# Kernel tuning notes

Hardware: AMD Instinct MI355X
Metric: run time of the kernel (lower is better)

Reference implementation:

```python
import jax, jax.numpy as jnp
import numpy as np
from jax import lax

FEAT_STRIDE = 16
PRE_NMS_TOP_N = 6000   # cfg['TEST'].RPN_PRE_NMS_TOP_N
POST_NMS_TOP_N = 300   # cfg['TEST'].RPN_POST_NMS_TOP_N
NMS_THRESH = 0.7       # cfg['TEST'].RPN_NMS_THRESH
MIN_SIZE = 16.0        # cfg['TEST'].RPN_MIN_SIZE
B, A, H, W = 32, 9, 128, 128
NEG_INF = jnp.float32(-1e30)


def _whctrs(a):
    w = a[2] - a[0] + 1.0
    h = a[3] - a[1] + 1.0
    return w, h, a[0] + 0.5 * (w - 1), a[1] + 0.5 * (h - 1)

def _mkanchors(ws, hs, xc, yc):
    ws = ws[:, None]; hs = hs[:, None]
    return np.hstack((xc - 0.5 * (ws - 1), yc - 0.5 * (hs - 1),
                      xc + 0.5 * (ws - 1), yc + 0.5 * (hs - 1)))

def _ratio_enum(anchor, ratios):
    w, h, xc, yc = _whctrs(anchor)
    size = w * h
    ws = np.round(np.sqrt(size / ratios))
    hs = np.round(ws * ratios)
    return _mkanchors(ws, hs, xc, yc)

def _scale_enum(anchor, scales):
    w, h, xc, yc = _whctrs(anchor)
    return _mkanchors(w * scales, h * scales, xc, yc)

def generate_anchors(base_size=16, ratios=np.array([0.5, 1.0, 2.0]), scales=np.array([8.0, 16.0, 32.0])):
    base = np.array([1, 1, base_size, base_size], dtype=np.float64) - 1
    ra = _ratio_enum(base, ratios)
    return np.vstack([_scale_enum(ra[i], scales) for i in range(ra.shape[0])]).astype(np.float32)

_BASE_ANCHORS = generate_anchors()  # (A, 4)

def _all_anchors(h, w):
    sx = np.arange(w) * FEAT_STRIDE
    sy = np.arange(h) * FEAT_STRIDE
    sx, sy = np.meshgrid(sx, sy)  # row-major (h, w) matches permute(0,2,3,1) ordering
    shifts = np.stack([sx.ravel(), sy.ravel(), sx.ravel(), sy.ravel()], axis=1).astype(np.float32)
    return jnp.asarray((shifts[:, None, :] + _BASE_ANCHORS[None, :, :]).reshape(-1, 4))  # (h*w*A, 4)

# ---- bbox_transform_inv / clip_boxes ----

def _decode(anchors, deltas):
    ws = anchors[:, 2] - anchors[:, 0] + 1.0
    hs = anchors[:, 3] - anchors[:, 1] + 1.0
    cx = anchors[:, 0] + 0.5 * ws
    cy = anchors[:, 1] + 0.5 * hs
    dx, dy, dw, dh = deltas[:, 0], deltas[:, 1], deltas[:, 2], deltas[:, 3]
    pcx = dx * ws + cx
    pcy = dy * hs + cy
    pw = jnp.exp(dw) * ws
    ph = jnp.exp(dh) * hs
    return jnp.stack([pcx - 0.5 * pw, pcy - 0.5 * ph, pcx + 0.5 * pw, pcy + 0.5 * ph], axis=1)

def _clip(b, imh, imw):
    x1 = jnp.clip(b[:, 0], 0.0, imw - 1.0)
    y1 = jnp.clip(b[:, 1], 0.0, imh - 1.0)
    x2 = jnp.clip(b[:, 2], 0.0, imw - 1.0)
    y2 = jnp.clip(b[:, 3], 0.0, imh - 1.0)
    return jnp.stack([x1, y1, x2, y2], axis=1)

# ---- greedy NMS: pick top-score box, suppress IoU > thresh, repeat POST times ----

def _nms_select(boxes, scores):
    # boxes: (PRE, 4) score-sorted; scores: (PRE,)
    areas = (boxes[:, 2] - boxes[:, 0] + 1.0) * (boxes[:, 3] - boxes[:, 1] + 1.0)

    def body(i, st):
        s, keep, valid = st
        j = jnp.argmax(s)
        keep = keep.at[i].set(j)
        valid = valid.at[i].set(s[j] > NEG_INF)
        b = boxes[j]
        xx1 = jnp.maximum(b[0], boxes[:, 0])
        yy1 = jnp.maximum(b[1], boxes[:, 1])
        xx2 = jnp.minimum(b[2], boxes[:, 2])
        yy2 = jnp.minimum(b[3], boxes[:, 3])
        inter = jnp.maximum(xx2 - xx1 + 1.0, 0.0) * jnp.maximum(yy2 - yy1 + 1.0, 0.0)
        iou = inter / jnp.maximum(areas[j] + areas - inter, 1e-6)
        s = jnp.where(iou > NMS_THRESH, NEG_INF, s)  # suppresses j itself (IoU = 1)
        return s, keep, valid

    init = (scores, jnp.zeros((POST_NMS_TOP_N,), jnp.int32), jnp.zeros((POST_NMS_TOP_N,), bool))
    _, keep, valid = lax.fori_loop(0, POST_NMS_TOP_N, body, init)
    return keep, valid

def _per_image(sc, dl, info, anchors):
    prop = _clip(_decode(anchors, dl), info[0], info[1])  # (K*A, 4)
    ws = prop[:, 2] - prop[:, 0] + 1.0
    hs = prop[:, 3] - prop[:, 1] + 1.0
    min_sz = MIN_SIZE * info[2]
    sc = jnp.where((ws >= min_sz) & (hs >= min_sz), sc, NEG_INF)
    top_s, top_i = lax.top_k(sc, PRE_NMS_TOP_N)
    cand = prop[top_i]  # (PRE, 4)
    keep, valid = _nms_select(cand, top_s)
    return cand[keep] * valid[:, None].astype(cand.dtype)  # zero-pad invalid rows

def _forward(rpn_cls_prob, rpn_bbox_pred, im_info):
    b, _, h, w = rpn_cls_prob.shape
    anchors = _all_anchors(h, w)
    scores = rpn_cls_prob[:, A:, :, :].transpose(0, 2, 3, 1).reshape(b, -1)  # (b, h*w*A)
    deltas = rpn_bbox_pred.transpose(0, 2, 3, 1).reshape(b, -1, 4)           # (b, h*w*A, 4)
    boxes = jax.vmap(lambda s, d, i: _per_image(s, d, i, anchors))(scores, deltas, im_info)
    ids = jnp.broadcast_to(jnp.arange(b, dtype=boxes.dtype)[:, None, None], (b, POST_NMS_TOP_N, 1))
    return jnp.concatenate([ids, boxes], axis=2)  # (b, POST, 5): [batch_idx, x1, y1, x2, y2]

def setup_inputs() -> dict:
    key = jax.random.key(0)
    k1, k2 = jax.random.split(key)
    rpn_cls_prob = jax.random.uniform(k1, (B, 2 * A, H, W), dtype=jnp.float32)
    rpn_bbox_pred = jax.random.normal(k2, (B, 4 * A, H, W), dtype=jnp.float32) * 0.2
    im_info = jnp.tile(jnp.array([[H * FEAT_STRIDE, W * FEAT_STRIDE, 1.0]], dtype=jnp.float32), (B, 1))
    return {"rpn_cls_prob": rpn_cls_prob, "rpn_bbox_pred": rpn_bbox_pred, "im_info": im_info}

def reference(rpn_cls_prob, rpn_bbox_pred, im_info):
    return _forward(rpn_cls_prob, rpn_bbox_pred, im_info)
```

## Files before the change

kernel.cpp:

```cpp
#include <hip/hip_runtime.h>
#include <cstdint>
#include <cstddef>

#pragma clang fp contract(off)

typedef unsigned long long u64;

#define NB 32
#define NA 9
#define NH 128
#define NW 128
#define HW (NH*NW)
#define NANCH (NA*HW)
#define PRE_N 6000
#define POST_N 300
#define CAND_CAP 8192
#define NMS_T 0.7f
#define GX_GATHER 24
#define NBOX 6144
#define CH 512

__constant__ float c_wa[9] = {184.f,368.f,736.f,128.f,256.f,512.f,88.f,176.f,352.f};
__constant__ float c_ha[9] = {96.f,192.f,384.f,128.f,256.f,512.f,176.f,352.f,704.f};

__device__ __forceinline__ float4 decode_clip(int a, int h, int w,
    float dx, float dy, float dlw, float dlh, float imh, float imw) {
  float wa = c_wa[a], ha = c_ha[a];
  float cx = (float)w * 16.0f + 8.0f;
  float cy = (float)h * 16.0f + 8.0f;
  float pcx = dx * wa + cx;
  float pcy = dy * ha + cy;
  float pw = expf(dlw) * wa;
  float ph = expf(dlh) * ha;
  float x1 = pcx - 0.5f * pw;
  float y1 = pcy - 0.5f * ph;
  float x2 = pcx + 0.5f * pw;
  float y2 = pcy + 0.5f * ph;
  float4 r;
  r.x = fminf(fmaxf(x1, 0.0f), imw - 1.0f);
  r.y = fminf(fmaxf(y1, 0.0f), imh - 1.0f);
  r.z = fminf(fmaxf(x2, 0.0f), imw - 1.0f);
  r.w = fminf(fmaxf(y2, 0.0f), imh - 1.0f);
  return r;
}

__device__ __forceinline__ unsigned score_key(float sc, float bw, float bh, float msz) {
  unsigned bits = __float_as_uint(sc);
  unsigned key = (bits & 0x80000000u) ? ~bits : (bits | 0x80000000u);
  if (!(bw >= msz && bh >= msz)) key = 0u;
  return key;
}

__device__ __forceinline__ bool sup_test4(float4 v, float ar, float4 p, float pa) {
  float xx1 = fmaxf(p.x, v.x), yy1 = fmaxf(p.y, v.y);
  float xx2 = fminf(p.z, v.z), yy2 = fminf(p.w, v.w);
  float iw = fmaxf(xx2 - xx1 + 1.0f, 0.0f);
  float ih = fmaxf(yy2 - yy1 + 1.0f, 0.0f);
  float inter = iw * ih;
  float iou = inter / fmaxf(pa + ar - inter, 1e-6f);
  return iou > NMS_T;
}

__device__ __forceinline__ u64 shfl_xor_u64(u64 x, int m) {
  int lo = __shfl_xor((int)(unsigned)x, m, 64);
  int hi = __shfl_xor((int)(unsigned)(x >> 32), m, 64);
  return ((u64)(unsigned)hi << 32) | (unsigned)lo;
}

__device__ __forceinline__ void reg_step(u64 v[8], int t, int k, int j) {
  #pragma unroll
  for (int r = 0; r < 8; ++r) {
    if ((r & j) == 0) {
      int e = (t << 3) + r;
      bool up = ((e & k) == 0);
      u64 x = v[r], y = v[r | j];
      u64 mx = x > y ? x : y, mn = x > y ? y : x;
      v[r]     = up ? mx : mn;
      v[r | j] = up ? mn : mx;
    }
  }
}

__device__ __forceinline__ void shfl_step(u64 v[8], int t, int k, int j) {
  int m = j >> 3;
  bool lower = ((t & m) == 0);
  #pragma unroll
  for (int r = 0; r < 8; ++r) {
    int e = (t << 3) + r;
    bool up = ((e & k) == 0);
    u64 pv = shfl_xor_u64(v[r], m);
    bool keepmax = (up == lower);
    u64 x = v[r];
    u64 mx = x > pv ? x : pv, mn = x > pv ? pv : x;
    v[r] = keepmax ? mx : mn;
  }
}

__device__ __forceinline__ void lds_step(u64* sm, u64 v[8], int t, int k, int j) {
  int m = j >> 3;
  __syncthreads();
  #pragma unroll
  for (int r = 0; r < 8; ++r) sm[(r << 10) | t] = v[r];
  __syncthreads();
  bool lower = ((t & m) == 0);
  bool up = (((t << 3) & k) == 0);
  bool keepmax = (up == lower);
  int pt = t ^ m;
  #pragma unroll
  for (int r = 0; r < 8; ++r) {
    u64 pv = sm[(r << 10) | pt];
    u64 x = v[r];
    u64 mx = x > pv ? x : pv, mn = x > pv ? pv : x;
    v[r] = keepmax ? mx : mn;
  }
}

__device__ void find_B(const unsigned* __restrict__ hb, unsigned* part,
                       unsigned* outB, unsigned* outCum) {
  int tid = threadIdx.x;
  unsigned s = 0;
  for (int i = 0; i < 16; ++i) s += hb[tid*16 + i];
  part[tid] = s;
  __syncthreads();
  for (int off = 1; off < 256; off <<= 1) {
    unsigned v = (tid + off < 256) ? part[tid + off] : 0u;
    __syncthreads();
    part[tid] += v;
    __syncthreads();
  }
  unsigned St = part[tid];
  unsigned Sn = (tid < 255) ? part[tid + 1] : 0u;
  if (St >= (unsigned)PRE_N && Sn < (unsigned)PRE_N) {
    unsigned cum = Sn, B = 0, cumAbove = Sn;
    for (int i = 15; i >= 0; --i) {
      unsigned v = hb[tid*16 + i];
      if (cum + v >= (unsigned)PRE_N) { B = (unsigned)(tid*16 + i); cumAbove = cum; break; }
      cum += v;
    }
    *outB = B; *outCum = cumAbove;
  }
  __syncthreads();
}

__device__ void find_thr(const unsigned* __restrict__ hb2, unsigned B, unsigned cum0,
                         unsigned* part, unsigned* outThr) {
  int tid = threadIdx.x;
  unsigned s = 0;
  for (int i = 0; i < 16; ++i) s += hb2[tid*16 + i];
  part[tid] = s;
  __syncthreads();
  for (int off = 1; off < 256; off <<= 1) {
    unsigned v = (tid + off < 256) ? part[tid + off] : 0u;
    __syncthreads();
    part[tid] += v;
    __syncthreads();
  }
  unsigned St = cum0 + part[tid];
  unsigned Sn = cum0 + ((tid < 255) ? part[tid + 1] : 0u);
  if (St >= (unsigned)PRE_N && Sn < (unsigned)PRE_N) {
    unsigned cum = Sn, t = 1u;
    for (int i = 15; i >= 0; --i) {
      unsigned v = hb2[tid*16 + i];
      if (cum + v >= (unsigned)PRE_N) {
        t = (B << 20) | ((unsigned)(tid*16 + i) << 8);
        break;
      }
      cum += v;
    }
    if (t == 0u) t = 1u;
    *outThr = t;
  }
  __syncthreads();
}

__global__ __launch_bounds__(256) void k_keys(const float* __restrict__ cls,
    const float* __restrict__ dl, const float* __restrict__ info,
    unsigned* __restrict__ keys, unsigned* __restrict__ hist) {
  __shared__ unsigned hsh[4096];
  int tid = threadIdx.x;
  for (int i = tid; i < 4096; i += 256) hsh[i] = 0;
  int t = blockIdx.x * 256 + tid;
  int b = blockIdx.y;
  int hw0 = t * 4;
  int h = hw0 >> 7;
  const float* dlb  = dl  + (size_t)b * (4*NA*HW);
  const float* clsb = cls + (size_t)b * (2*NA*HW);
  float imh = info[b*3+0], imw = info[b*3+1];
  float msz = 16.0f * info[b*3+2];
  unsigned* kb = keys + (size_t)b * NANCH;
  __syncthreads();
  #pragma unroll
  for (int a = 0; a < 9; ++a) {
    float4 dx4 = *(const float4*)&dlb[(a*4+0)*HW + hw0];
    float4 dy4 = *(const float4*)&dlb[(a*4+1)*HW + hw0];
    float4 dw4 = *(const float4*)&dlb[(a*4+2)*HW + hw0];
    float4 dh4 = *(const float4*)&dlb[(a*4+3)*HW + hw0];
    float4 sc4 = *(const float4*)&clsb[(NA+a)*HW + hw0];
    uint4 out;
    {
      float4 bx = decode_clip(a, h, (hw0+0)&127, dx4.x, dy4.x, dw4.x, dh4.x, imh, imw);
      out.x = score_key(sc4.x, bx.z-bx.x+1.0f, bx.w-bx.y+1.0f, msz);
    }
    {
      float4 bx = decode_clip(a, h, (hw0+1)&127, dx4.y, dy4.y, dw4.y, dh4.y, imh, imw);
      out.y = score_key(sc4.y, bx.z-bx.x+1.0f, bx.w-bx.y+1.0f, msz);
    }
    {
      float4 bx = decode_clip(a, h, (hw0+2)&127, dx4.z, dy4.z, dw4.z, dh4.z, imh, imw);
      out.z = score_key(sc4.z, bx.z-bx.x+1.0f, bx.w-bx.y+1.0f, msz);
    }
    {
      float4 bx = decode_clip(a, h, (hw0+3)&127, dx4.w, dy4.w, dw4.w, dh4.w, imh, imw);
      out.w = score_key(sc4.w, bx.z-bx.x+1.0f, bx.w-bx.y+1.0f, msz);
    }
    *(uint4*)&kb[a*HW + hw0] = out;
    atomicAdd(&hsh[out.x >> 20], 1u);
    atomicAdd(&hsh[out.y >> 20], 1u);
    atomicAdd(&hsh[out.z >> 20], 1u);
    atomicAdd(&hsh[out.w >> 20], 1u);
  }
  __syncthreads();
  unsigned* gb = hist + ((size_t)b << 12);
  for (int i = tid; i < 4096; i += 256) {
    unsigned v = hsh[i];
    if (v) atomicAdd(&gb[i], v);
  }
}

__global__ __launch_bounds__(256) void k_hist2(const unsigned* __restrict__ keys,
    const unsigned* __restrict__ hist1, unsigned* __restrict__ hist2) {
  __shared__ unsigned h[4096];
  __shared__ unsigned part[256];
  __shared__ unsigned sB, sCum;
  int b = blockIdx.y, tid = threadIdx.x;
  for (int i = tid; i < 4096; i += 256) h[i] = 0;
  __syncthreads();
  find_B(hist1 + ((size_t)b << 12), part, &sB, &sCum);
  unsigned B = sB;
  const unsigned* kb = keys + (size_t)b * NANCH;
  for (int i = blockIdx.x * 256 + tid; i < NANCH; i += gridDim.x * 256) {
    unsigned k = kb[i];
    if ((k >> 20) == B) atomicAdd(&h[(k >> 8) & 4095u], 1u);
  }
  __syncthreads();
  unsigned* gb = hist2 + ((size_t)b << 12);
  for (int i = tid; i < 4096; i += 256) { unsigned v = h[i]; if (v) atomicAdd(&gb[i], v); }
}

__global__ __launch_bounds__(256) void k_gather(const unsigned* __restrict__ keys,
    const unsigned* __restrict__ hist1, const unsigned* __restrict__ hist2,
    const float* __restrict__ dl, const float* __restrict__ info,
    unsigned* __restrict__ cnt, u64* __restrict__ cand,
    float4* __restrict__ boxes) {
  int b = blockIdx.y, tid = threadIdx.x;
  int lane = tid & 63, wv = tid >> 6;
  __shared__ unsigned part[256];
  __shared__ unsigned sB, sCum, sThr;
  __shared__ unsigned wcnt[4], woff[4], blkbase;
  if (tid == 0) sThr = 1u;
  __syncthreads();
  find_B(hist1 + ((size_t)b << 12), part, &sB, &sCum);
  find_thr(hist2 + ((size_t)b << 12), sB, sCum, part, &sThr);
  unsigned t_ = sThr;
  const unsigned* kb = keys + (size_t)b * NANCH;
  const float* dlb = dl + (size_t)b * (4*NA*HW);
  float imh = info[b*3+0], imw = info[b*3+1];
  u64* cb = cand + (size_t)b * CAND_CAP;
  float4* bxc = boxes + (size_t)b * CAND_CAP;
  unsigned* cp = cnt + (size_t)b * 64;
  const int PER_BLK = NANCH / GX_GATHER;
  int base0 = blockIdx.x * PER_BLK;
  for (int it = 0; it < PER_BLK / 256; ++it) {
    int j = base0 + it * 256 + tid;
    unsigned key = kb[j];
    bool pass = key >= t_;
    u64 mask = __ballot(pass);
    if (lane == 0) wcnt[wv] = (unsigned)__popcll(mask);
    __syncthreads();
    if (tid == 0) {
      unsigned s0 = 0;
      for (int w = 0; w < 4; ++w) { woff[w] = s0; s0 += wcnt[w]; }
      blkbase = s0 ? atomicAdd(cp, s0) : 0u;
    }
    __syncthreads();
    if (pass) {
      unsigned pos = blkbase + woff[wv] + (unsigned)__popcll(mask & ((1ull << lane) - 1ull));
      if (pos < CAND_CAP) {
        int a = j >> 14, hw = j & (HW - 1);
        unsigned oi = (unsigned)(hw * 9 + a);
        unsigned noi = (~oi) & 0x3FFFFu;
        cb[pos] = ((u64)key << 32) | ((u64)noi << 13) | (u64)pos;
        bxc[pos] = decode_clip(a, hw >> 7, hw & 127,
                               dlb[(a*4+0)*HW + hw], dlb[(a*4+1)*HW + hw],
                               dlb[(a*4+2)*HW + hw], dlb[(a*4+3)*HW + hw],
                               imh, imw);
      }
    }
    __syncthreads();
  }
}

__global__ __launch_bounds__(1024) void k_final5(const u64* __restrict__ cand,
    const unsigned* __restrict__ cnt, const float4* __restrict__ boxes,
    float* __restrict__ out) {
  __shared__ float4 bx[NBOX];
  __shared__ float4 cbox2[CH];
  __shared__ float  carea2[CH];
  __shared__ float4 kbox[POST_N];
  __shared__ float  karea[POST_N];
  __shared__ u64 sup[CH][9];
  __shared__ u64 aliveM[8];
  __shared__ u64 kgW[8];
  __shared__ int s_nk;
  u64* sm = (u64*)bx;

  int b = blockIdx.x, tid = threadIdx.x;
  int lane = tid & 63, wv = tid >> 6;
  if (tid == 0) s_nk = 0;

  unsigned effcnt = cnt[b * 64];
  if (effcnt > CAND_CAP) effcnt = CAND_CAP;
  const u64* cb = cand + (size_t)b * CAND_CAP;
  int e0 = tid << 3;
  u64 v[8];
  #pragma unroll
  for (int r = 0; r < 8; ++r)
    v[r] = ((unsigned)(e0 + r) < effcnt) ? cb[e0 + r] : 0ull;

  for (int k = 2; k <= 8; k <<= 1)
    for (int j = k >> 1; j >= 1; j >>= 1) reg_step(v, tid, k, j);
  for (int k = 16; k <= CAND_CAP; k <<= 1) {
    int j = k >> 1;
    for (; j >= 512; j >>= 1) lds_step(sm, v, tid, k, j);
    for (; j >= 8;   j >>= 1) shfl_step(v, tid, k, j);
    for (; j >= 1;   j >>= 1) reg_step(v, tid, k, j);
  }
  __syncthreads();

  const float4* bxc = boxes + (size_t)b * CAND_CAP;
  #pragma unroll
  for (int r = 0; r < 8; ++r) {
    int rank = e0 + r;
    if (rank < NBOX) {
      u64 ck = (rank < PRE_N) ? v[r] : 0ull;
      float4 w = make_float4(0.f, 0.f, -1.f, -1.f);
      if ((unsigned)(ck >> 32) != 0u)
        w = bxc[(unsigned)(ck & 0x1FFFu)];
      bx[rank] = w;
    }
  }
  __syncthreads();

  float* ob = out + (size_t)b * (POST_N * 5);
  int c = tid & (CH - 1);
  int seg = tid >> 9;

  for (int base = 0; base < NBOX; base += CH) {
    int nk0 = s_nk;

    bool alive = false;
    float4 w; float ar = 0.f;
    if (tid < CH) {
      w = bx[base + tid];
      float wid = w.z - w.x + 1.0f;
      alive = wid > 0.0f;
      ar = wid * (w.w - w.y + 1.0f);
      if (alive) {
        for (int k = 0; k < nk0; ++k) {
          if (sup_test4(w, ar, kbox[k], karea[k])) { alive = false; break; }
        }
      }
      u64 am = __ballot(alive);
      if (lane == 0) aliveM[wv] = am;
    }
    __syncthreads();

    int na = 0;
    #pragma unroll
    for (int g = 0; g < 8; ++g) na += (int)__popcll(aliveM[g]);
    if (na == 0) continue;

    if (tid < CH && alive) {
      int cg2 = tid >> 6;
      int pre = 0;
      #pragma unroll
      for (int g = 0; g < 8; ++g) if (g < cg2) pre += (int)__popcll(aliveM[g]);
      pre += (int)__popcll(aliveM[cg2] & ((1ull << (tid & 63)) - 1ull));
      cbox2[pre] = w;
      carea2[pre] = ar;
    }
    __syncthreads();

    {
      int i = c;
      if (i < na) {
        int ngi = (i >> 6) + 1;
        int gA = seg ? (ngi >> 1) : 0;
        int gB = seg ? ngi : (ngi >> 1);
        if (gA < gB) {
          float4 vi = cbox2[i];
          float ai = carea2[i];
          for (int g = gA; g < gB; ++g) {
            int jmax = i - (g << 6);
            if (jmax > 64) jmax = 64;
            u64 r = 0;
            #pragma unroll 4
            for (int j = 0; j < jmax; ++j) {
              if (sup_test4(vi, ai, cbox2[(g << 6) + j], carea2[(g << 6) + j]))
                r |= 1ull << j;
            }
            sup[i][g] = r;
          }
        }
      }
    }
    __syncthreads();

    if (tid < 64) {
      u64 kw[8];
      int nst = (na + 63) >> 6;
      u64 srow[8];
      {
        const u64* rp = sup[lane];
        #pragma unroll
        for (int g = 0; g < 8; ++g) srow[g] = rp[g];
      }
      #pragma unroll
      for (int s = 0; s < 8; ++s) {
        u64 nsr[8];
        bool pf = (s + 1 < nst);
        if (pf) {
          const u64* rp = sup[(s + 1) * 64 + lane];
          #pragma unroll
          for (int g = 0; g < 8; ++g) nsr[g] = rp[g];
        }
        u64 kg = 0;
        if (s < nst) {
          int cc = s * 64 + lane;
          bool a = (cc < na);
          u64 blocked = 0;
          #pragma unroll
          for (int g = 0; g < 8; ++g) if (g < s) blocked |= (srow[g] & kw[g]);
          a = a && (blocked == 0ull);
          u64 r = a ? srow[s] : 0ull;
          u64 cm = __ballot(a);
          while (cm) {
            int j = __builtin_ctzll(cm);
            kg |= 1ull << j;
            u64 rem = __ballot((r >> j) & 1ull);
            cm &= ~(rem | (1ull << j));
          }
        }
        kw[s] = kg;
        if (pf) {
          #pragma unroll
          for (int g = 0; g < 8; ++g) srow[g] = nsr[g];
        }
      }
      if (lane == 0) {
        #pragma unroll
        for (int s = 0; s < 8; ++s) kgW[s] = kw[s];
      }
    }
    __syncthreads();

    if (tid < na) {
      int s = tid >> 6;
      u64 kgw = kgW[s];
      bool kept = (kgw >> (tid & 63)) & 1;
      int pre = 0;
      #pragma unroll
      for (int g = 0; g < 8; ++g) if (g < s) pre += (int)__popcll(kgW[g]);
      pre += (int)__popcll(kgw & ((1ull << (tid & 63)) - 1ull));
      int rank = nk0 + pre;
      if (kept && rank < POST_N) {
        float4 ww = cbox2[tid];
        kbox[rank] = ww; karea[rank] = carea2[tid];
        ob[rank*5+0] = (float)b;
        ob[rank*5+1] = ww.x; ob[rank*5+2] = ww.y; ob[rank*5+3] = ww.z; ob[rank*5+4] = ww.w;
      }
    }
    if (tid == 0) {
      int tot = 0;
      #pragma unroll
      for (int s = 0; s < 8; ++s) tot += (int)__popcll(kgW[s]);
      int nn = nk0 + tot;
      s_nk = nn < POST_N ? nn : POST_N;
    }
    __syncthreads();
    if (s_nk >= POST_N) break;
  }
  __syncthreads();
  int nk = s_nk;
  for (int r = nk + tid; r < POST_N; r += 1024) {
    ob[r*5+0] = (float)b;
    ob[r*5+1] = 0.f; ob[r*5+2] = 0.f; ob[r*5+3] = 0.f; ob[r*5+4] = 0.f;
  }
}

extern "C" void kernel_launch(void* const* d_in, const int* in_sizes, int n_in,
                              void* d_out, int out_size, void* d_ws, size_t ws_size,
                              hipStream_t stream) {
  const float* cls  = (const float*)d_in[0];
  const float* dl   = (const float*)d_in[1];
  const float* info = (const float*)d_in[2];
  float* out = (float*)d_out;
  char* ws = (char*)d_ws;

  const size_t OFF_KEYS = 0;
  const size_t OFF_H1   = 18874368;
  const size_t OFF_H2   = 19398656;
  const size_t OFF_CNT  = 19922944;
  const size_t OFF_CAND = 19931136;
  const size_t OFF_BOX  = 22028288;
  const size_t WS_NEED  = 26222592;
  if (ws_size < WS_NEED) return;

  unsigned* keys  = (unsigned*)(ws + OFF_KEYS);
  unsigned* h1    = (unsigned*)(ws + OFF_H1);
  unsigned* h2    = (unsigned*)(ws + OFF_H2);
  unsigned* cnt   = (unsigned*)(ws + OFF_CNT);
  u64* cand = (u64*)(ws + OFF_CAND);
  float4* boxes = (float4*)(ws + OFF_BOX);

  hipMemsetAsync(ws + OFF_H1, 0, OFF_CAND - OFF_H1, stream);

  dim3 g1(HW / 1024, NB);
  k_keys<<<g1, 256, 0, stream>>>(cls, dl, info, keys, h1);
  dim3 gh(8, NB);
  k_hist2<<<gh, 256, 0, stream>>>(keys, h1, h2);
  dim3 gg(GX_GATHER, NB);
  k_gather<<<gg, 256, 0, stream>>>(keys, h1, h2, dl, info, cnt, cand, boxes);
  k_final5<<<NB, 1024, 0, stream>>>(cand, cnt, boxes, out);
}
```

Measured before the change: 330.5 us.

## Eagerly suppress future NMS chunks against newly kept boxes across all threads

The chunked NMS kernel used to test each 512-box chunk against every previously kept box serially, and only 512 threads did that work. Now each of the 1024 threads holds 6 candidate boxes in registers with a dead mask. After each chunk, all threads test their future boxes only against the boxes just kept, so the suppression work is spread over the whole block and is incremental. The cost is more registers per thread (six float4 boxes plus areas), which may cause spilling at 1024 threads, and redundant tests on boxes that would never be reached once 300 are kept.

```diff
diff --git a/kernel.cpp b/kernel.cpp
--- a/kernel.cpp
+++ b/kernel.cpp
@@ -300,7 +300,7 @@
   }
 }
 
-__global__ __launch_bounds__(1024) void k_final5(const u64* __restrict__ cand,
+__global__ __launch_bounds__(1024) void k_final6(const u64* __restrict__ cand,
     const unsigned* __restrict__ cnt, const float4* __restrict__ boxes,
     float* __restrict__ out) {
   __shared__ float4 bx[NBOX];
@@ -351,144 +351,170 @@
   }
   __syncthreads();
 
+  float4 mybx[6];
+  float  myar[6];
+  int deadm = 0;
+  #pragma unroll
+  for (int m = 0; m < 6; ++m) {
+    float4 w = bx[tid + (m << 10)];
+    mybx[m] = w;
+    float wid = w.z - w.x + 1.0f;
+    myar[m] = wid * (w.w - w.y + 1.0f);
+    if (!(wid > 0.0f)) deadm |= (1 << m);
+  }
+
   float* ob = out + (size_t)b * (POST_N * 5);
-  int c = tid & (CH - 1);
+  int c512 = tid & (CH - 1);
   int seg = tid >> 9;
-
-  for (int base = 0; base < NBOX; base += CH) {
-    int nk0 = s_nk;
-
-    bool alive = false;
-    float4 w; float ar = 0.f;
-    if (tid < CH) {
-      w = bx[base + tid];
-      float wid = w.z - w.x + 1.0f;
-      alive = wid > 0.0f;
-      ar = wid * (w.w - w.y + 1.0f);
+  bool done = false;
+
+  #pragma unroll
+  for (int m = 0; m < 6; ++m) {
+    #pragma unroll
+    for (int par = 0; par < 2; ++par) {
+      if (done) continue;
+      int nk0 = s_nk;
+
+      bool own = (tid >> 9) == par;
+      int cc = tid - (par << 9);
+      bool alive = own && !((deadm >> m) & 1);
+      {
+        u64 am = __ballot(alive);
+        if (own && lane == 0) aliveM[wv & 7] = am;
+      }
+      __syncthreads();
+
+      int na = 0;
+      #pragma unroll
+      for (int g = 0; g < 8; ++g) na += (int)__popcll(aliveM[g]);
+      if (na == 0) continue;
+
       if (alive) {
-        for (int k = 0; k < nk0; ++k) {
-          if (sup_test4(w, ar, kbox[k], karea[k])) { alive = false; break; }
-        }
-      }
-      u64 am = __ballot(alive);
-      if (lane == 0) aliveM[wv] = am;
-    }
-    __syncthreads();
-
-    int na = 0;
-    #pragma unroll
-    for (int g = 0; g < 8; ++g) na += (int)__popcll(aliveM[g]);
-    if (na == 0) continue;
-
-    if (tid < CH && alive) {
-      int cg2 = tid >> 6;
-      int pre = 0;
-      #pragma unroll
-      for (int g = 0; g < 8; ++g) if (g < cg2) pre += (int)__popcll(aliveM[g]);
-      pre += (int)__popcll(aliveM[cg2] & ((1ull << (tid & 63)) - 1ull));
-      cbox2[pre] = w;
-      carea2[pre] = ar;
-    }
-    __syncthreads();
-
-    {
-      int i = c;
-      if (i < na) {
-        int ngi = (i >> 6) + 1;
-        int gA = seg ? (ngi >> 1) : 0;
-        int gB = seg ? ngi : (ngi >> 1);
-        if (gA < gB) {
-          float4 vi = cbox2[i];
-          float ai = carea2[i];
-          for (int g = gA; g < gB; ++g) {
-            int jmax = i - (g << 6);
-            if (jmax > 64) jmax = 64;
-            u64 r = 0;
-            #pragma unroll 4
-            for (int j = 0; j < jmax; ++j) {
-              if (sup_test4(vi, ai, cbox2[(g << 6) + j], carea2[(g << 6) + j]))
-                r |= 1ull << j;
+        int cg2 = cc >> 6;
+        int pre = 0;
+        #pragma unroll
+        for (int g = 0; g < 8; ++g) if (g < cg2) pre += (int)__popcll(aliveM[g]);
+        pre += (int)__popcll(aliveM[cg2] & ((1ull << (cc & 63)) - 1ull));
+        cbox2[pre] = mybx[m];
+        carea2[pre] = myar[m];
+      }
+      __syncthreads();
+
+      {
+        int i = c512;
+        if (i < na) {
+          int ngi = (i >> 6) + 1;
+          int gA = seg ? (ngi >> 1) : 0;
+          int gB = seg ? ngi : (ngi >> 1);
+          if (gA < gB) {
+            float4 vi = cbox2[i];
+            float ai = carea2[i];
+            for (int g = gA; g < gB; ++g) {
+              int jmax = i - (g << 6);
+              if (jmax > 64) jmax = 64;
+              u64 r = 0;
+              #pragma unroll 4
+              for (int j = 0; j < jmax; ++j) {
+                if (sup_test4(vi, ai, cbox2[(g << 6) + j], carea2[(g << 6) + j]))
+                  r |= 1ull << j;
+              }
+              sup[i][g] = r;
             }
-            sup[i][g] = r;
           }
         }
       }
-    }
-    __syncthreads();
-
-    if (tid < 64) {
-      u64 kw[8];
-      int nst = (na + 63) >> 6;
-      u64 srow[8];
-      {
-        const u64* rp = sup[lane];
+      __syncthreads();
+
+      if (tid < 64) {
+        u64 kw[8];
+        int nst = (na + 63) >> 6;
+        u64 srow[8];
+        {
+          const u64* rp = sup[lane];
+          #pragma unroll
+          for (int g = 0; g < 8; ++g) srow[g] = rp[g];
+        }
         #pragma unroll
-        for (int g = 0; g < 8; ++g) srow[g] = rp[g];
-      }
-      #pragma unroll
-      for (int s = 0; s < 8; ++s) {
-        u64 nsr[8];
-        bool pf = (s + 1 < nst);
-        if (pf) {
-          const u64* rp = sup[(s + 1) * 64 + lane];
-          #pragma unroll
-          for (int g = 0; g < 8; ++g) nsr[g] = rp[g];
-        }
-        u64 kg = 0;
-        if (s < nst) {
-          int cc = s * 64 + lane;
-          bool a = (cc < na);
-          u64 blocked = 0;
-          #pragma unroll
-          for (int g = 0; g < 8; ++g) if (g < s) blocked |= (srow[g] & kw[g]);
-          a = a && (blocked == 0ull);
-          u64 r = a ? srow[s] : 0ull;
-          u64 cm = __ballot(a);
-          while (cm) {
-            int j = __builtin_ctzll(cm);
-            kg |= 1ull << j;
-            u64 rem = __ballot((r >> j) & 1ull);
-            cm &= ~(rem | (1ull << j));
+        for (int s = 0; s < 8; ++s) {
+          u64 nsr[8];
+          bool pf = (s + 1 < nst);
+          if (pf) {
+            const u64* rp = sup[(s + 1) * 64 + lane];
+            #pragma unroll
+            for (int g = 0; g < 8; ++g) nsr[g] = rp[g];
+          }
+          u64 kg = 0;
+          if (s < nst) {
+            int cc2 = s * 64 + lane;
+            bool a = (cc2 < na);
+            u64 blocked = 0;
+            #pragma unroll
+            for (int g = 0; g < 8; ++g) if (g < s) blocked |= (srow[g] & kw[g]);
+            a = a && (blocked == 0ull);
+            u64 r = a ? srow[s] : 0ull;
+            u64 cm = __ballot(a);
+            while (cm) {
+              int j = __builtin_ctzll(cm);
+              kg |= 1ull << j;
+              u64 rem = __ballot((r >> j) & 1ull);
+              cm &= ~(rem | (1ull << j));
+            }
+          }
+          kw[s] = kg;
+          if (pf) {
+            #pragma unroll
+            for (int g = 0; g < 8; ++g) srow[g] = nsr[g];
           }
         }
-        kw[s] = kg;
-        if (pf) {
+        if (lane == 0) {
           #pragma unroll
-          for (int g = 0; g < 8; ++g) srow[g] = nsr[g];
+          for (int s = 0; s < 8; ++s) kgW[s] = kw[s];
         }
       }
-      if (lane == 0) {
+      __syncthreads();
+
+      if (tid < na) {
+        int s = tid >> 6;
+        u64 kgw = kgW[s];
+        bool kept = (kgw >> (tid & 63)) & 1;
+        int pre = 0;
         #pragma unroll
-        for (int s = 0; s < 8; ++s) kgW[s] = kw[s];
-      }
-    }
-    __syncthreads();
-
-    if (tid < na) {
-      int s = tid >> 6;
-      u64 kgw = kgW[s];
-      bool kept = (kgw >> (tid & 63)) & 1;
-      int pre = 0;
-      #pragma unroll
-      for (int g = 0; g < 8; ++g) if (g < s) pre += (int)__popcll(kgW[g]);
-      pre += (int)__popcll(kgw & ((1ull << (tid & 63)) - 1ull));
-      int rank = nk0 + pre;
-      if (kept && rank < POST_N) {
-        float4 ww = cbox2[tid];
-        kbox[rank] = ww; karea[rank] = carea2[tid];
-        ob[rank*5+0] = (float)b;
-        ob[rank*5+1] = ww.x; ob[rank*5+2] = ww.y; ob[rank*5+3] = ww.z; ob[rank*5+4] = ww.w;
-      }
-    }
-    if (tid == 0) {
-      int tot = 0;
-      #pragma unroll
-      for (int s = 0; s < 8; ++s) tot += (int)__popcll(kgW[s]);
-      int nn = nk0 + tot;
-      s_nk = nn < POST_N ? nn : POST_N;
-    }
-    __syncthreads();
-    if (s_nk >= POST_N) break;
+        for (int g = 0; g < 8; ++g) if (g < s) pre += (int)__popcll(kgW[g]);
+        pre += (int)__popcll(kgw & ((1ull << (tid & 63)) - 1ull));
+        int rank = nk0 + pre;
+        if (kept && rank < POST_N) {
+          float4 ww = cbox2[tid];
+          kbox[rank] = ww; karea[rank] = carea2[tid];
+          ob[rank*5+0] = (float)b;
+          ob[rank*5+1] = ww.x; ob[rank*5+2] = ww.y; ob[rank*5+3] = ww.z; ob[rank*5+4] = ww.w;
+        }
+      }
+      if (tid == 0) {
+        int tot = 0;
+        #pragma unroll
+        for (int s = 0; s < 8; ++s) tot += (int)__popcll(kgW[s]);
+        int nn = nk0 + tot;
+        s_nk = nn < POST_N ? nn : POST_N;
+      }
+      __syncthreads();
+
+      int nk1 = s_nk;
+      if (nk1 >= POST_N) { done = true; continue; }
+      if (nk1 > nk0) {
+        #pragma unroll
+        for (int m2 = m; m2 < 6; ++m2) {
+          bool fut = (m2 > m) || ((tid >> 9) > par);
+          if (fut && !((deadm >> m2) & 1)) {
+            for (int k = nk0; k < nk1; ++k) {
+              if (sup_test4(mybx[m2], myar[m2], kbox[k], karea[k])) {
+                deadm |= (1 << m2);
+                break;
+              }
+            }
+          }
+        }
+      }
+    }
   }
   __syncthreads();
   int nk = s_nk;
@@ -531,5 +557,5 @@
   k_hist2<<<gh, 256, 0, stream>>>(keys, h1, h2);
   dim3 gg(GX_GATHER, NB);
   k_gather<<<gg, 256, 0, stream>>>(keys, h1, h2, dl, info, cnt, cand, boxes);
-  k_final5<<<NB, 1024, 0, stream>>>(cand, cnt, boxes, out);
-}
+  k_final6<<<NB, 1024, 0, stream>>>(cand, cnt, boxes, out);
+}
```

New measurement: 337.5 us. +2.1%, slower.
